# Optimization experiments

Hardware: AMD Instinct MI355X
Metric: run time of the kernel (lower is better)

Reference implementation:

```python
import jax, jax.numpy as jnp
import numpy as np

K = 3
PAD = 1
EPS = 1e-5


def _unfold(x, k, pad):
    # torch.nn.Unfold(k, dilation=1, padding=pad, stride=1): output [B, C*k*k, L]
    # with channel-major ordering (c, ki, kj) in the second dim.
    B, C, H, W = x.shape
    xp = jnp.pad(x, ((0, 0), (0, 0), (pad, pad), (pad, pad)))
    Ho = H + 2 * pad - k + 1
    Wo = W + 2 * pad - k + 1
    patches = jnp.stack(
        [xp[:, :, i:i + Ho, j:j + Wo] for i in range(k) for j in range(k)],
        axis=2,
    )  # [B, C, k*k, Ho, Wo]
    return patches.reshape(B, C * k * k, Ho * Wo)


def _conv1x1(x, w, b):
    return jnp.einsum('bchw,oc->bohw', x, w) + b[None, :, None, None]


def _bn(x, g, b):
    # training-mode BatchNorm2d: batch stats over (B,H,W), biased variance
    mu = x.mean(axis=(0, 2, 3), keepdims=True)
    var = x.var(axis=(0, 2, 3), keepdims=True)
    return (x - mu) * jax.lax.rsqrt(var + EPS) * g[None, :, None, None] + b[None, :, None, None]


def _tri(x, w, b, g, be):
    return jax.nn.relu(_bn(_conv1x1(x, w, b), g, be))


def reference(x, w1, b1, g1, be1, w2, b2, g2, be2, wf, bf, gf, bef):
    B, C, H, W = x.shape
    k2 = K * K
    c = k2 // 2
    tri1 = _tri(x, w1, b1, g1, be1)  # key map  [B,C,H,W] (m=1)
    tri2 = _tri(x, w2, b2, g2, be2)  # query map
    # NOTE: faithful to source: plain row-major reshape of [B, C*k2, L] -> [B, C, L, k2]
    ku = _unfold(tri1, K, PAD).reshape(B, C, -1, k2)
    qu = _unfold(tri2, K, PAD).reshape(B, C, -1, k2)
    logits = ku * qu[..., c:c + 1] + ku[..., c:c + 1] * qu
    dl_weight = jax.nn.softmax(logits, axis=-1)[:, None]  # [B,1,C,L,k2]
    xu = _unfold(x, K, PAD).reshape(B, 1, C, -1, k2)       # m=1 -> [B,1,C,L,k2]
    # NOTE: faithful to source: row-major reshape to [B, C, k2, L], sum over axis -2
    pre = (dl_weight * xu).reshape(B, C, k2, -1).sum(axis=-2).reshape(B, C, H, W)
    return jax.nn.relu(_bn(_conv1x1(pre, wf, bf), gf, bef))


def setup_inputs() -> dict:
    key = jax.random.key(0)
    B, C, O, H, W = 4, 256, 256, 64, 64
    ks = jax.random.split(key, 4)
    s = 1.0 / np.sqrt(C)
    return {
        'x': jax.random.normal(ks[0], (B, C, H, W), dtype=jnp.float32),
        'w1': jax.random.normal(ks[1], (C, C), dtype=jnp.float32) * s,
        'b1': jnp.zeros((C,), jnp.float32),
        'g1': jnp.ones((C,), jnp.float32),
        'be1': jnp.zeros((C,), jnp.float32),
        'w2': jax.random.normal(ks[2], (C, C), dtype=jnp.float32) * s,
        'b2': jnp.zeros((C,), jnp.float32),
        'g2': jnp.ones((C,), jnp.float32),
        'be2': jnp.zeros((C,), jnp.float32),
        'wf': jax.random.normal(ks[3], (O, C), dtype=jnp.float32) * s,
        'bf': jnp.zeros((O,), jnp.float32),
        'gf': jnp.ones((O,), jnp.float32),
        'bef': jnp.zeros((O,), jnp.float32),
    }
```

## Files before the change

### kernel.cpp

```cpp
#include <hip/hip_runtime.h>
#include <hip/hip_bf16.h>

#define L 4096
#define CCH 256
#define NB 4
#define KP 40
#define GOF 72
#define LOG2E 1.4426950408889634f

typedef __attribute__((ext_vector_type(8))) short short8;
typedef __attribute__((ext_vector_type(4))) float f32x4;
typedef unsigned short ushort_t;

__device__ __forceinline__ unsigned short f2bf(float f) {
    unsigned u = __builtin_bit_cast(unsigned, f);
    u += 0x7FFF + ((u >> 16) & 1);
    return (unsigned short)(u >> 16);
}
__device__ __forceinline__ unsigned pk_bf16(float a, float b) {
    __hip_bfloat162 h = __float22bfloat162_rn(make_float2(a, b));
    unsigned u;
    __builtin_memcpy(&u, &h, 4);
    return u;
}
__device__ __forceinline__ float bflo(unsigned w) {
    return __builtin_bit_cast(float, w << 16);
}
__device__ __forceinline__ float bfhi(unsigned w) {
    return __builtin_bit_cast(float, w & 0xFFFF0000u);
}
__device__ __forceinline__ float bfu(ushort_t h) {
    return __builtin_bit_cast(float, (unsigned)h << 16);
}

__global__ __launch_bounds__(256) void wcvt_k(
    const float* __restrict__ w1, const float* __restrict__ w2,
    const float* __restrict__ wf,
    ushort_t* __restrict__ wb1, ushort_t* __restrict__ wb2,
    ushort_t* __restrict__ wbf)
{
    const int mb = blockIdx.x >> 6;
    const int i  = (blockIdx.x & 63) * 256 + threadIdx.x;
    const float* src = (mb == 0) ? w1 : (mb == 1) ? w2 : wf;
    ushort_t*    dst = (mb == 0) ? wb1 : (mb == 1) ? wb2 : wbf;
    float4 v = ((const float4*)src)[i];
    uint2 p;
    p.x = pk_bf16(v.x, v.y);
    p.y = pk_bf16(v.z, v.w);
    ((uint2*)dst)[i] = p;
}

__global__ __launch_bounds__(256, 2) void dual_gemm_k(
    const float* __restrict__ x,
    const ushort_t* __restrict__ wb1, const float* __restrict__ b1,
    const ushort_t* __restrict__ wb2, const float* __restrict__ b2,
    ushort_t* __restrict__ y1, ushort_t* __restrict__ y2)
{
    __shared__ short sA1[128 * KP];
    __shared__ short sA2[128 * KP];
    __shared__ short sB [64 * KP];

    const int tid = threadIdx.x;
    const int l0 = blockIdx.x * 64;
    const int o0 = blockIdx.y * 128;
    const int b  = blockIdx.z;

    const int wv = tid >> 6;
    const int lane = tid & 63;
    const int m = lane & 15;
    const int quad = lane >> 4;

    const float* xb = x + (size_t)b * CCH * L;

    const int sl = tid & 63, soct = tid >> 6;
    const int sr = tid & 127, sh = tid >> 7;

    f32x4 acc1[2][4], acc2[2][4];
    #pragma unroll
    for (int io = 0; io < 2; ++io)
        #pragma unroll
        for (int jl = 0; jl < 4; ++jl) {
            acc1[io][jl] = (f32x4){0.f,0.f,0.f,0.f};
            acc2[io][jl] = (f32x4){0.f,0.f,0.f,0.f};
        }

    for (int s = 0; s < 8; ++s) {
        const int k0 = s * 32;
        __syncthreads();
        {
            const float* xs = xb + (size_t)(k0 + soct * 8) * L + l0 + sl;
            float f[8];
            #pragma unroll
            for (int j = 0; j < 8; ++j) f[j] = xs[(size_t)j * L];
            uint4 v;
            v.x = pk_bf16(f[0], f[1]);
            v.y = pk_bf16(f[2], f[3]);
            v.z = pk_bf16(f[4], f[5]);
            v.w = pk_bf16(f[6], f[7]);
            *(uint4*)&sB[sl * KP + soct * 8] = v;
        }
        {
            const uint4* wp = (const uint4*)&wb1[(size_t)(o0 + sr) * CCH + k0 + sh * 16];
            uint4 p0 = wp[0], p1 = wp[1];
            *(uint4*)&sA1[sr * KP + sh * 16]     = p0;
            *(uint4*)&sA1[sr * KP + sh * 16 + 8] = p1;
            const uint4* wq = (const uint4*)&wb2[(size_t)(o0 + sr) * CCH + k0 + sh * 16];
            uint4 q0 = wq[0], q1 = wq[1];
            *(uint4*)&sA2[sr * KP + sh * 16]     = q0;
            *(uint4*)&sA2[sr * KP + sh * 16 + 8] = q1;
        }
        __syncthreads();
        short8 a1[2], a2[2], bf[4];
        #pragma unroll
        for (int io = 0; io < 2; ++io) {
            a1[io] = *(const short8*)&sA1[(wv * 32 + io * 16 + m) * KP + quad * 8];
            a2[io] = *(const short8*)&sA2[(wv * 32 + io * 16 + m) * KP + quad * 8];
        }
        #pragma unroll
        for (int jl = 0; jl < 4; ++jl)
            bf[jl] = *(const short8*)&sB[(jl * 16 + m) * KP + quad * 8];
        #pragma unroll
        for (int io = 0; io < 2; ++io)
            #pragma unroll
            for (int jl = 0; jl < 4; ++jl) {
                acc1[io][jl] = __builtin_amdgcn_mfma_f32_16x16x32_bf16(a1[io], bf[jl], acc1[io][jl], 0, 0, 0);
                acc2[io][jl] = __builtin_amdgcn_mfma_f32_16x16x32_bf16(a2[io], bf[jl], acc2[io][jl], 0, 0, 0);
            }
    }

    #pragma unroll
    for (int io = 0; io < 2; ++io)
        #pragma unroll
        for (int reg = 0; reg < 4; ++reg) {
            const int o = o0 + wv * 32 + io * 16 + quad * 4 + reg;
            const float bb1 = b1[o], bb2 = b2[o];
            const size_t ro = ((size_t)b * CCH + o) * L + l0 + m;
            unsigned u1a = pk_bf16(acc1[io][0][reg] + bb1, acc1[io][1][reg] + bb1);
            unsigned u1b = pk_bf16(acc1[io][2][reg] + bb1, acc1[io][3][reg] + bb1);
            unsigned u2a = pk_bf16(acc2[io][0][reg] + bb2, acc2[io][1][reg] + bb2);
            unsigned u2b = pk_bf16(acc2[io][2][reg] + bb2, acc2[io][3][reg] + bb2);
            y1[ro]      = (ushort_t)u1a;
            y1[ro + 16] = (ushort_t)(u1a >> 16);
            y1[ro + 32] = (ushort_t)u1b;
            y1[ro + 48] = (ushort_t)(u1b >> 16);
            y2[ro]      = (ushort_t)u2a;
            y2[ro + 16] = (ushort_t)(u2a >> 16);
            y2[ro + 32] = (ushort_t)u2b;
            y2[ro + 48] = (ushort_t)(u2b >> 16);
        }
}

__global__ __launch_bounds__(256, 2) void single_gemm_k(
    const ushort_t* __restrict__ x,
    const ushort_t* __restrict__ wb, const float* __restrict__ bb,
    ushort_t* __restrict__ y)
{
    __shared__ short sA[128 * KP];
    __shared__ short sB[64 * KP];

    const int tid = threadIdx.x;
    const int l0 = blockIdx.x * 64;
    const int o0 = blockIdx.y * 128;
    const int b  = blockIdx.z;

    const int wv = tid >> 6;
    const int lane = tid & 63;
    const int m = lane & 15;
    const int quad = lane >> 4;

    const ushort_t* xb = x + (size_t)b * CCH * L;

    const int sl = tid & 63, soct = tid >> 6;
    const int sr = tid & 127, sh = tid >> 7;

    f32x4 acc[2][4];
    #pragma unroll
    for (int io = 0; io < 2; ++io)
        #pragma unroll
        for (int jl = 0; jl < 4; ++jl)
            acc[io][jl] = (f32x4){0.f,0.f,0.f,0.f};

    for (int s = 0; s < 8; ++s) {
        const int k0 = s * 32;
        __syncthreads();
        {
            const ushort_t* xs = xb + (size_t)(k0 + soct * 8) * L + l0 + sl;
            short8 v;
            #pragma unroll
            for (int j = 0; j < 8; ++j) v[j] = (short)xs[(size_t)j * L];
            *(short8*)&sB[sl * KP + soct * 8] = v;
        }
        {
            const uint4* wp = (const uint4*)&wb[(size_t)(o0 + sr) * CCH + k0 + sh * 16];
            uint4 p0 = wp[0], p1 = wp[1];
            *(uint4*)&sA[sr * KP + sh * 16]     = p0;
            *(uint4*)&sA[sr * KP + sh * 16 + 8] = p1;
        }
        __syncthreads();
        short8 a[2], bf[4];
        #pragma unroll
        for (int io = 0; io < 2; ++io)
            a[io] = *(const short8*)&sA[(wv * 32 + io * 16 + m) * KP + quad * 8];
        #pragma unroll
        for (int jl = 0; jl < 4; ++jl)
            bf[jl] = *(const short8*)&sB[(jl * 16 + m) * KP + quad * 8];
        #pragma unroll
        for (int io = 0; io < 2; ++io)
            #pragma unroll
            for (int jl = 0; jl < 4; ++jl)
                acc[io][jl] = __builtin_amdgcn_mfma_f32_16x16x32_bf16(a[io], bf[jl], acc[io][jl], 0, 0, 0);
    }

    #pragma unroll
    for (int io = 0; io < 2; ++io)
        #pragma unroll
        for (int reg = 0; reg < 4; ++reg) {
            const int o = o0 + wv * 32 + io * 16 + quad * 4 + reg;
            const float b0 = bb[o];
            const size_t ro = ((size_t)b * CCH + o) * L + l0 + m;
            unsigned ua = pk_bf16(acc[io][0][reg] + b0, acc[io][1][reg] + b0);
            unsigned ub = pk_bf16(acc[io][2][reg] + b0, acc[io][3][reg] + b0);
            y[ro]      = (ushort_t)ua;
            y[ro + 16] = (ushort_t)(ua >> 16);
            y[ro + 32] = (ushort_t)ub;
            y[ro + 48] = (ushort_t)(ub >> 16);
        }
}

__device__ __forceinline__ void bn_stats_body(
    const ushort_t* y, const float* gamma, const float* beta,
    float* scale, float* shift, int c, int tid, float kscale)
{
    float s = 0.f, s2 = 0.f;
    for (int b = 0; b < NB; ++b) {
        const uint4* p = (const uint4*)(y + ((size_t)b * CCH + c) * L);
        #pragma unroll
        for (int r = 0; r < 2; ++r) {
            uint4 v = p[r * 256 + tid];
            unsigned w[4] = {v.x, v.y, v.z, v.w};
            #pragma unroll
            for (int u = 0; u < 4; ++u) {
                float a = bflo(w[u]), bb = bfhi(w[u]);
                s  += a + bb;
                s2 += a * a + bb * bb;
            }
        }
    }
    #pragma unroll
    for (int off = 32; off > 0; off >>= 1) {
        s  += __shfl_down(s, off);
        s2 += __shfl_down(s2, off);
    }
    __shared__ float red[2][4];
    if ((tid & 63) == 0) { red[0][tid >> 6] = s; red[1][tid >> 6] = s2; }
    __syncthreads();
    if (tid == 0) {
        float S  = red[0][0] + red[0][1] + red[0][2] + red[0][3];
        float S2 = red[1][0] + red[1][1] + red[1][2] + red[1][3];
        const float invN = 1.f / (NB * (float)L);
        float mean = S * invN;
        float var  = S2 * invN - mean * mean;
        float rstd = rsqrtf(var + 1e-5f);
        float g = gamma[c];
        scale[c] = kscale * g * rstd;
        shift[c] = kscale * (beta[c] - mean * g * rstd);
    }
}

__global__ __launch_bounds__(256) void bn_stats2_k(
    const ushort_t* __restrict__ y1, const float* __restrict__ g1, const float* __restrict__ be1,
    float* __restrict__ sc1, float* __restrict__ sh1,
    const ushort_t* __restrict__ y2, const float* __restrict__ g2, const float* __restrict__ be2,
    float* __restrict__ sc2, float* __restrict__ sh2)
{
    const int c = blockIdx.x & 255;
    if (blockIdx.x < 256) bn_stats_body(y1, g1, be1, sc1, sh1, c, threadIdx.x, LOG2E);
    else                  bn_stats_body(y2, g2, be2, sc2, sh2, c, threadIdx.x, 1.0f);
}

__global__ __launch_bounds__(512, 4) void attention_k(
    const float* __restrict__ x,
    const ushort_t* __restrict__ y1,
    const ushort_t* __restrict__ y2,
    const float* __restrict__ s1sc, const float* __restrict__ s1sh,
    const float* __restrict__ s2sc, const float* __restrict__ s2sh,
    ushort_t* __restrict__ pre)
{
    __shared__ unsigned sKQg[4240];
    __shared__ ushort_t sXg [4240];
    __shared__ uint2    sCI [L];

    const int bc = blockIdx.x;
    const int tid = threadIdx.x;
    const int ch = bc & 255;
    const size_t off = (size_t)bc * L;

    const float sc1 = s1sc[ch], sh1 = s1sh[ch];
    const float sc2 = s2sc[ch], sh2 = s2sh[ch];

    if (tid < GOF)  { sKQg[tid] = 0; sXg[tid] = 0; }
    if (tid < 72)   { sKQg[GOF + 4096 + tid] = 0; sXg[GOF + 4096 + tid] = 0; }
    {
        uint4 ak = ((const uint4*)(y1 + off))[tid];
        uint4 aq = ((const uint4*)(y2 + off))[tid];
        float4 xa = ((const float4*)(x + off))[2 * tid];
        float4 xb = ((const float4*)(x + off))[2 * tid + 1];
        unsigned wk[4] = {ak.x, ak.y, ak.z, ak.w};
        unsigned wq[4] = {aq.x, aq.y, aq.z, aq.w};
        unsigned kq[8];
        #pragma unroll
        for (int u = 0; u < 4; ++u) {
            float klo = fmaxf(fmaf(bflo(wk[u]), sc1, sh1), 0.f);
            float khi = fmaxf(fmaf(bfhi(wk[u]), sc1, sh1), 0.f);
            float qlo = fmaxf(fmaf(bflo(wq[u]), sc2, sh2), 0.f);
            float qhi = fmaxf(fmaf(bfhi(wq[u]), sc2, sh2), 0.f);
            kq[2*u]   = (unsigned)f2bf(klo) | ((unsigned)f2bf(qlo) << 16);
            kq[2*u+1] = (unsigned)f2bf(khi) | ((unsigned)f2bf(qhi) << 16);
        }
        *(uint4*)&sKQg[GOF + 8 * tid]     = make_uint4(kq[0], kq[1], kq[2], kq[3]);
        *(uint4*)&sKQg[GOF + 8 * tid + 4] = make_uint4(kq[4], kq[5], kq[6], kq[7]);
        float xv[8] = {xa.x, xa.y, xa.z, xa.w, xb.x, xb.y, xb.z, xb.w};
        unsigned xp[4];
        #pragma unroll
        for (int u = 0; u < 4; ++u)
            xp[u] = (unsigned)f2bf(xv[2*u]) | ((unsigned)f2bf(xv[2*u+1]) << 16);
        *(uint4*)&sXg[GOF + 8 * tid] = make_uint4(xp[0], xp[1], xp[2], xp[3]);
    }
    __syncthreads();

    {
        const int fbase = 9 * tid;
        #pragma unroll
        for (int r = 0; r < 8; ++r) {
            const int f  = fbase + 4608 * r;
            const int t  = f >> 12;
            const int fl = f & 4095;
            unsigned wv[9];
            if (fl < 4088) {
                const int di = (t * 86) >> 8;
                const int dj = t - 3 * di;
                const int cbad = (dj == 0) ? 0 : ((dj == 2) ? 63 : 99);
                const int base = fl + (di << 6) + dj - 65 + GOF;
                #pragma unroll
                for (int j = 0; j < 9; ++j) wv[j] = sKQg[base + j];
                #pragma unroll
                for (int j = 0; j < 9; ++j) {
                    int c = (fl + j) & 63;
                    wv[j] = (c == cbad) ? 0u : wv[j];
                }
            } else {
                #pragma unroll
                for (int j = 0; j < 9; ++j) {
                    int fj = f + j;
                    int tj = fj >> 12, lj = fj & 4095;
                    int dij = (tj * 86) >> 8, djj = tj - 3 * dij;
                    int idx = lj + (dij << 6) + djj - 65 + GOF;
                    unsigned wr = sKQg[idx];
                    int c = lj & 63;
                    int cb = (djj == 0) ? 0 : ((djj == 2) ? 63 : 99);
                    wv[j] = (c == cb) ? 0u : wr;
                }
            }
            const unsigned cw = wv[4];
            const float kc = bflo(cw), qc = bfhi(cw);
            float e0 = __builtin_amdgcn_exp2f(bflo(wv[0]) * qc + kc * bfhi(wv[0]));
            float e1 = __builtin_amdgcn_exp2f(bflo(wv[1]) * qc + kc * bfhi(wv[1]));
            float e2 = __builtin_amdgcn_exp2f(bflo(wv[2]) * qc + kc * bfhi(wv[2]));
            float e3 = __builtin_amdgcn_exp2f(bflo(wv[3]) * qc + kc * bfhi(wv[3]));
            float e4 = __builtin_amdgcn_exp2f(bflo(wv[4]) * qc + kc * bfhi(wv[4]));
            float e5 = __builtin_amdgcn_exp2f(bflo(wv[5]) * qc + kc * bfhi(wv[5]));
            float e6 = __builtin_amdgcn_exp2f(bflo(wv[6]) * qc + kc * bfhi(wv[6]));
            float e7 = __builtin_amdgcn_exp2f(bflo(wv[7]) * qc + kc * bfhi(wv[7]));
            float e8 = __builtin_amdgcn_exp2f(bflo(wv[8]) * qc + kc * bfhi(wv[8]));
            float s = (((e0 + e1) + (e2 + e3)) + ((e4 + e5) + (e6 + e7))) + e8;
            uint2 ci;
            ci.x = cw;
            ci.y = __builtin_bit_cast(unsigned, -__builtin_amdgcn_logf(s));
            sCI[r * 512 + tid] = ci;
        }
    }
    __syncthreads();

    {
        const int c0 = tid & 63;
        float acc[8];
        #pragma unroll
        for (int r = 0; r < 8; ++r) acc[r] = 0.f;

        #pragma unroll
        for (int t = 0; t < 9; ++t) {
            const int di = t / 3, dj = t % 3;
            const int base = tid + (di << 6) + dj - 65 + GOF;
            const bool colbad = (dj == 0) ? (c0 == 0) : ((dj == 2) ? (c0 == 63) : false);
            const int ft = (t << 12) + tid;
            #pragma unroll
            for (int r = 0; r < 8; ++r) {
                const int f = ft + 512 * r;
                const unsigned lp = (unsigned)f / 9u;
                uint2 ci = sCI[lp];
                const float kc = bflo(ci.x), qc = bfhi(ci.x);
                const float cn = __builtin_bit_cast(float, ci.y);
                unsigned wv = sKQg[base + 512 * r];
                float xj = bfu(sXg[base + 512 * r]);
                xj = colbad ? 0.f : xj;
                float e = __builtin_amdgcn_exp2f(fmaf(bflo(wv), qc, fmaf(kc, bfhi(wv), cn)));
                acc[r] = fmaf(e, xj, acc[r]);
            }
        }
        #pragma unroll
        for (int r = 0; r < 8; ++r)
            pre[off + r * 512 + tid] = f2bf(acc[r]);
    }
}

__global__ __launch_bounds__(256) void bn_fused_k(
    const ushort_t* __restrict__ yf,
    const float* __restrict__ gf, const float* __restrict__ bef,
    float* __restrict__ out)
{
    __shared__ uint4 sY[2048];
    __shared__ float red[2][4];
    __shared__ float fsc, fsh;

    const int c = blockIdx.x, tid = threadIdx.x;
    float s = 0.f, s2 = 0.f;
    #pragma unroll
    for (int b = 0; b < NB; ++b) {
        const uint4* p = (const uint4*)(yf + ((size_t)b * CCH + c) * L);
        #pragma unroll
        for (int r = 0; r < 2; ++r) {
            uint4 v = p[r * 256 + tid];
            sY[b * 512 + r * 256 + tid] = v;
            unsigned w[4] = {v.x, v.y, v.z, v.w};
            #pragma unroll
            for (int u = 0; u < 4; ++u) {
                float a = bflo(w[u]), bb = bfhi(w[u]);
                s  += a + bb;
                s2 += a * a + bb * bb;
            }
        }
    }
    #pragma unroll
    for (int off = 32; off > 0; off >>= 1) {
        s  += __shfl_down(s, off);
        s2 += __shfl_down(s2, off);
    }
    if ((tid & 63) == 0) { red[0][tid >> 6] = s; red[1][tid >> 6] = s2; }
    __syncthreads();
    if (tid == 0) {
        float S  = red[0][0] + red[0][1] + red[0][2] + red[0][3];
        float S2 = red[1][0] + red[1][1] + red[1][2] + red[1][3];
        const float invN = 1.f / (NB * (float)L);
        float mean = S * invN;
        float var  = S2 * invN - mean * mean;
        float rstd = rsqrtf(var + 1e-5f);
        float g = gf[c];
        fsc = g * rstd;
        fsh = bef[c] - mean * g * rstd;
    }
    __syncthreads();
    const float sc = fsc, sh = fsh;

    #pragma unroll
    for (int b = 0; b < NB; ++b) {
        float4* o = (float4*)(out + ((size_t)b * CCH + c) * L);
        #pragma unroll
        for (int r = 0; r < 2; ++r) {
            uint4 v = sY[b * 512 + r * 256 + tid];
            unsigned w[4] = {v.x, v.y, v.z, v.w};
            float4 o0, o1;
            o0.x = fmaxf(fmaf(bflo(w[0]), sc, sh), 0.f);
            o0.y = fmaxf(fmaf(bfhi(w[0]), sc, sh), 0.f);
            o0.z = fmaxf(fmaf(bflo(w[1]), sc, sh), 0.f);
            o0.w = fmaxf(fmaf(bfhi(w[1]), sc, sh), 0.f);
            o1.x = fmaxf(fmaf(bflo(w[2]), sc, sh), 0.f);
            o1.y = fmaxf(fmaf(bfhi(w[2]), sc, sh), 0.f);
            o1.z = fmaxf(fmaf(bflo(w[3]), sc, sh), 0.f);
            o1.w = fmaxf(fmaf(bfhi(w[3]), sc, sh), 0.f);
            int i = r * 256 + tid;
            o[2 * i]     = o0;
            o[2 * i + 1] = o1;
        }
    }
}

extern "C" void kernel_launch(void* const* d_in, const int* in_sizes, int n_in,
                              void* d_out, int out_size, void* d_ws, size_t ws_size,
                              hipStream_t stream) {
    const float* x   = (const float*)d_in[0];
    const float* w1  = (const float*)d_in[1];
    const float* b1  = (const float*)d_in[2];
    const float* g1  = (const float*)d_in[3];
    const float* be1 = (const float*)d_in[4];
    const float* w2  = (const float*)d_in[5];
    const float* b2  = (const float*)d_in[6];
    const float* g2  = (const float*)d_in[7];
    const float* be2 = (const float*)d_in[8];
    const float* wf  = (const float*)d_in[9];
    const float* bf  = (const float*)d_in[10];
    const float* gf  = (const float*)d_in[11];
    const float* bef = (const float*)d_in[12];
    float* out = (float*)d_out;

    const size_t NEL = (size_t)NB * CCH * L;
    ushort_t* y1b = (ushort_t*)d_ws;
    ushort_t* y2b = y1b + NEL;
    float* st = (float*)(y2b + NEL);
    float* s1sc = st,        *s1sh = st + 256;
    float* s2sc = st + 512,  *s2sh = st + 768;
    ushort_t* wb1 = (ushort_t*)(st + 1536);
    ushort_t* wb2 = wb1 + CCH * CCH;
    ushort_t* wbf = wb2 + CCH * CCH;

    wcvt_k<<<192, 256, 0, stream>>>(w1, w2, wf, wb1, wb2, wbf);
    dim3 gg(64, 2, 4);
    dual_gemm_k<<<gg, 256, 0, stream>>>(x, wb1, b1, wb2, b2, y1b, y2b);
    bn_stats2_k<<<512, 256, 0, stream>>>(y1b, g1, be1, s1sc, s1sh,
                                         y2b, g2, be2, s2sc, s2sh);
    attention_k<<<NB * CCH, 512, 0, stream>>>(x, y1b, y2b,
                                              s1sc, s1sh, s2sc, s2sh,
                                              y2b);
    single_gemm_k<<<gg, 256, 0, stream>>>(y2b, wbf, bf, y1b);
    bn_fused_k<<<256, 256, 0, stream>>>(y1b, gf, bef, out);
}
```

Baseline: 158.7 us.

## Scatter softmax-weighted x into LDS via atomics instead of recomputing exps

```diff
diff --git a/kernel.cpp b/kernel.cpp
--- a/kernel.cpp
+++ b/kernel.cpp
@@ -278,7 +278,7 @@
     else                  bn_stats_body(y2, g2, be2, sc2, sh2, c, threadIdx.x, 1.0f);
 }
 
-__global__ __launch_bounds__(512, 4) void attention_k(
+__global__ __launch_bounds__(512, 6) void attention_k(
     const float* __restrict__ x,
     const ushort_t* __restrict__ y1,
     const ushort_t* __restrict__ y2,
@@ -288,7 +288,7 @@
 {
     __shared__ unsigned sKQg[4240];
     __shared__ ushort_t sXg [4240];
-    __shared__ uint2    sCI [L];
+    __shared__ float    accF[L];
 
     const int bc = blockIdx.x;
     const int tid = threadIdx.x;
@@ -300,6 +300,11 @@
 
     if (tid < GOF)  { sKQg[tid] = 0; sXg[tid] = 0; }
     if (tid < 72)   { sKQg[GOF + 4096 + tid] = 0; sXg[GOF + 4096 + tid] = 0; }
+    {
+        float4 z = {0.f, 0.f, 0.f, 0.f};
+        ((float4*)accF)[tid]       = z;
+        ((float4*)accF)[tid + 512] = z;
+    }
     {
         uint4 ak = ((const uint4*)(y1 + off))[tid];
         uint4 aq = ((const uint4*)(y2 + off))[tid];
@@ -336,17 +341,23 @@
             const int t  = f >> 12;
             const int fl = f & 4095;
             unsigned wv[9];
+            float    xw[9];
             if (fl < 4088) {
                 const int di = (t * 86) >> 8;
                 const int dj = t - 3 * di;
                 const int cbad = (dj == 0) ? 0 : ((dj == 2) ? 63 : 99);
                 const int base = fl + (di << 6) + dj - 65 + GOF;
                 #pragma unroll
-                for (int j = 0; j < 9; ++j) wv[j] = sKQg[base + j];
+                for (int j = 0; j < 9; ++j) {
+                    wv[j] = sKQg[base + j];
+                    xw[j] = bfu(sXg[base + j]);
+                }
                 #pragma unroll
                 for (int j = 0; j < 9; ++j) {
                     int c = (fl + j) & 63;
-                    wv[j] = (c == cbad) ? 0u : wv[j];
+                    bool bad = (c == cbad);
+                    wv[j] = bad ? 0u  : wv[j];
+                    xw[j] = bad ? 0.f : xw[j];
                 }
             } else {
                 #pragma unroll
@@ -356,60 +367,43 @@
                     int dij = (tj * 86) >> 8, djj = tj - 3 * dij;
                     int idx = lj + (dij << 6) + djj - 65 + GOF;
                     unsigned wr = sKQg[idx];
+                    float    xr = bfu(sXg[idx]);
                     int c = lj & 63;
                     int cb = (djj == 0) ? 0 : ((djj == 2) ? 63 : 99);
-                    wv[j] = (c == cb) ? 0u : wr;
+                    bool bad = (c == cb);
+                    wv[j] = bad ? 0u  : wr;
+                    xw[j] = bad ? 0.f : xr;
                 }
             }
             const unsigned cw = wv[4];
             const float kc = bflo(cw), qc = bfhi(cw);
-            float e0 = __builtin_amdgcn_exp2f(bflo(wv[0]) * qc + kc * bfhi(wv[0]));
-            float e1 = __builtin_amdgcn_exp2f(bflo(wv[1]) * qc + kc * bfhi(wv[1]));
-            float e2 = __builtin_amdgcn_exp2f(bflo(wv[2]) * qc + kc * bfhi(wv[2]));
-            float e3 = __builtin_amdgcn_exp2f(bflo(wv[3]) * qc + kc * bfhi(wv[3]));
-            float e4 = __builtin_amdgcn_exp2f(bflo(wv[4]) * qc + kc * bfhi(wv[4]));
-            float e5 = __builtin_amdgcn_exp2f(bflo(wv[5]) * qc + kc * bfhi(wv[5]));
-            float e6 = __builtin_amdgcn_exp2f(bflo(wv[6]) * qc + kc * bfhi(wv[6]));
-            float e7 = __builtin_amdgcn_exp2f(bflo(wv[7]) * qc + kc * bfhi(wv[7]));
-            float e8 = __builtin_amdgcn_exp2f(bflo(wv[8]) * qc + kc * bfhi(wv[8]));
-            float s = (((e0 + e1) + (e2 + e3)) + ((e4 + e5) + (e6 + e7))) + e8;
-            uint2 ci;
-            ci.x = cw;
-            ci.y = __builtin_bit_cast(unsigned, -__builtin_amdgcn_logf(s));
-            sCI[r * 512 + tid] = ci;
+            float e[9];
+            #pragma unroll
+            for (int j = 0; j < 9; ++j)
+                e[j] = __builtin_amdgcn_exp2f(bflo(wv[j]) * qc + kc * bfhi(wv[j]));
+            float s = (((e[0] + e[1]) + (e[2] + e[3])) +
+                       ((e[4] + e[5]) + (e[6] + e[7]))) + e[8];
+            const float rinv = __builtin_amdgcn_rcpf(s);
+            if (fl < 4088) {
+                #pragma unroll
+                for (int j = 0; j < 9; ++j)
+                    atomicAdd(&accF[fl + j], e[j] * rinv * xw[j]);
+            } else {
+                #pragma unroll
+                for (int j = 0; j < 9; ++j)
+                    atomicAdd(&accF[(f + j) & 4095], e[j] * rinv * xw[j]);
+            }
         }
     }
     __syncthreads();
 
     {
-        const int c0 = tid & 63;
-        float acc[8];
-        #pragma unroll
-        for (int r = 0; r < 8; ++r) acc[r] = 0.f;
-
-        #pragma unroll
-        for (int t = 0; t < 9; ++t) {
-            const int di = t / 3, dj = t % 3;
-            const int base = tid + (di << 6) + dj - 65 + GOF;
-            const bool colbad = (dj == 0) ? (c0 == 0) : ((dj == 2) ? (c0 == 63) : false);
-            const int ft = (t << 12) + tid;
-            #pragma unroll
-            for (int r = 0; r < 8; ++r) {
-                const int f = ft + 512 * r;
-                const unsigned lp = (unsigned)f / 9u;
-                uint2 ci = sCI[lp];
-                const float kc = bflo(ci.x), qc = bfhi(ci.x);
-                const float cn = __builtin_bit_cast(float, ci.y);
-                unsigned wv = sKQg[base + 512 * r];
-                float xj = bfu(sXg[base + 512 * r]);
-                xj = colbad ? 0.f : xj;
-                float e = __builtin_amdgcn_exp2f(fmaf(bflo(wv), qc, fmaf(kc, bfhi(wv), cn)));
-                acc[r] = fmaf(e, xj, acc[r]);
-            }
-        }
-        #pragma unroll
-        for (int r = 0; r < 8; ++r)
-            pre[off + r * 512 + tid] = f2bf(acc[r]);
+        unsigned* po = (unsigned*)(pre + off);
+        #pragma unroll
+        for (int rr = 0; rr < 4; ++rr) {
+            const int p = rr * 512 + tid;
+            po[p] = pk_bf16(accF[2 * p], accF[2 * p + 1]);
+        }
     }
 }
 
```

New measurement: 328.6 us. +107.1%, slower.
